# Optimization experiments

Hardware: AMD Instinct MI355X
Metric: run time of the kernel (lower is better)

Reference implementation:

```python
import jax, jax.numpy as jnp
import numpy as np

N_NODES = 100000
N_EDGES = 3200000
EMB = 128
HID = 128
N_CLASS = 10
N_SHAPE = 16
N_COLOR = 16
MAX_POS = 150000
N_GRAPH = 1024


def setup_inputs() -> dict:
    key = jax.random.key(0)
    ks = jax.random.split(key, 12)
    node_feats = jax.random.randint(ks[0], (N_NODES, 3), 0, N_SHAPE, dtype=jnp.int64 if jax.config.jax_enable_x64 else jnp.int32)
    edge_index = jax.random.randint(ks[1], (2, N_EDGES), 0, N_NODES)
    batch = jnp.sort(jax.random.randint(ks[2], (N_NODES,), 0, N_GRAPH))
    s = 0.02
    shape_emb = jax.random.normal(ks[3], (N_SHAPE, EMB), jnp.float32) * s
    color_emb = jax.random.normal(ks[4], (N_COLOR, EMB), jnp.float32) * s
    pos_emb = jax.random.normal(ks[5], (MAX_POS, EMB), jnp.float32) * s
    w1_l = jax.random.normal(ks[6], (HID, EMB), jnp.float32) / np.sqrt(EMB)
    b1_l = jnp.zeros((HID,), jnp.float32)
    w1_r = jax.random.normal(ks[7], (HID, EMB), jnp.float32) / np.sqrt(EMB)
    w2_l = jax.random.normal(ks[8], (HID, HID), jnp.float32) / np.sqrt(HID)
    b2_l = jnp.zeros((HID,), jnp.float32)
    w2_r = jax.random.normal(ks[9], (HID, HID), jnp.float32) / np.sqrt(HID)
    lin_w = jax.random.normal(ks[10], (N_CLASS, HID), jnp.float32) / np.sqrt(HID)
    lin_b = jnp.zeros((N_CLASS,), jnp.float32)
    return {"node_feats": node_feats, "edge_index": edge_index, "batch": batch,
            "shape_emb": shape_emb, "color_emb": color_emb, "pos_emb": pos_emb,
            "w1_l": w1_l, "b1_l": b1_l, "w1_r": w1_r,
            "w2_l": w2_l, "b2_l": b2_l, "w2_r": w2_r,
            "lin_w": lin_w, "lin_b": lin_b}


def _sage_conv(x, src, dst, deg_inv, w_l, b_l, w_r):
    # mean-aggregate neighbor features: gather x[src], scatter-add at dst, divide by degree
    msg_sum = jax.ops.segment_sum(x[src], dst, num_segments=N_NODES)  # [N, D]
    agg = msg_sum * deg_inv[:, None]
    # PyG SAGEConv: lin_l(aggr) + lin_r(x); bias lives in lin_l
    return agg @ w_l.T + b_l + x @ w_r.T


def reference(node_feats, edge_index, batch, shape_emb, color_emb, pos_emb,
              w1_l, b1_l, w1_r, w2_l, b2_l, w2_r, lin_w, lin_b):
    s, c, p = node_feats[:, 0], node_feats[:, 1], node_feats[:, 2]
    x = shape_emb[s] + color_emb[c] + pos_emb[p]            # [N, EMB]
    src, dst = edge_index[0], edge_index[1]
    deg = jax.ops.segment_sum(jnp.ones((N_EDGES,), x.dtype), dst, num_segments=N_NODES)
    deg_inv = jnp.where(deg > 0, 1.0 / jnp.maximum(deg, 1.0), 0.0)
    x = jax.nn.relu(_sage_conv(x, src, dst, deg_inv, w1_l, b1_l, w1_r))
    x = jax.nn.relu(_sage_conv(x, src, dst, deg_inv, w2_l, b2_l, w2_r))
    # global mean pool over graphs
    pooled_sum = jax.ops.segment_sum(x, batch, num_segments=N_GRAPH)  # [G, HID]
    counts = jax.ops.segment_sum(jnp.ones((N_NODES,), x.dtype), batch, num_segments=N_GRAPH)
    pooled = pooled_sum / jnp.maximum(counts, 1.0)[:, None]
    return pooled @ lin_w.T + lin_b                          # [G, N_CLASS]
```

## Files before the change

kernel.cpp:

```cpp
#include <hip/hip_runtime.h>

#define N_NODES 100000
#define N_EDGES 3200000
#define EMB 128
#define N_GRAPH 1024
#define N_CLASS 10
#define CAP 96

#define EPB 1280
#define NBLK_E (N_EDGES / EPB)
#define NBK 391
#define NTOT (NBK * NBLK_E)
#define SCAN_B 1024
#define NB_SCAN ((NTOT + SCAN_B - 1) / SCAN_B)

#define EMBED_BLKS (N_NODES * 16 / 256)
#define WCAT_BLKS 256

typedef unsigned int uint32;
typedef __attribute__((ext_vector_type(8))) short bf16x8;
typedef __attribute__((ext_vector_type(4))) float f32x4;
typedef __attribute__((ext_vector_type(2))) float f32x2;

__device__ inline unsigned short f2bf(float f) {
  unsigned u = __float_as_uint(f);
  u += 0x7fffu + ((u >> 16) & 1u);
  return (unsigned short)(u >> 16);
}
__device__ inline float bf2f(unsigned short s) {
  return __uint_as_float(((unsigned)s) << 16);
}
__device__ inline unsigned char f2fp8(float v) {
  return (unsigned char)(__builtin_amdgcn_cvt_pk_fp8_f32(v, v, 0, false) & 0xff);
}

__global__ __launch_bounds__(256) void k_hist(
    const int* __restrict__ dst, int* __restrict__ counts,
    const int* __restrict__ nf, const float* __restrict__ se,
    const float* __restrict__ ce, const float* __restrict__ pe,
    unsigned short* __restrict__ X, unsigned char* __restrict__ X8,
    const float* __restrict__ w1l, const float* __restrict__ w1r,
    const float* __restrict__ w2l, const float* __restrict__ w2r,
    unsigned short* __restrict__ wc1, unsigned short* __restrict__ wc2) {
  int b = blockIdx.x;
  int tid = threadIdx.x;
  if (b < NBLK_E) {
    __shared__ int h[NBK];
    for (int i = tid; i < NBK; i += 256) h[i] = 0;
    __syncthreads();
    int base = b * EPB;
#pragma unroll
    for (int it = 0; it < 5; ++it) {
      int d = dst[base + it * 256 + tid];
      atomicAdd(&h[d >> 8], 1);
    }
    __syncthreads();
    for (int i = tid; i < NBK; i += 256) counts[i * NBLK_E + b] = h[i];
  } else if (b < NBLK_E + EMBED_BLKS) {
    int gid = (b - NBLK_E) * 256 + tid;
    int node = gid >> 4;
    int q = (gid & 15) * 8;
    int s = nf[node * 3 + 0];
    int c = nf[node * 3 + 1];
    int p = nf[node * 3 + 2];
    const float* ps = se + s * EMB + q;
    const float* pc = ce + c * EMB + q;
    const float* pp = pe + p * EMB + q;
    float4 a0 = *(const float4*)ps, a1 = *(const float4*)(ps + 4);
    float4 b0 = *(const float4*)pc, b1 = *(const float4*)(pc + 4);
    float4 d0 = *(const float4*)pp, d1 = *(const float4*)(pp + 4);
    float r0 = a0.x + b0.x + d0.x, r1 = a0.y + b0.y + d0.y;
    float r2 = a0.z + b0.z + d0.z, r3 = a0.w + b0.w + d0.w;
    float r4 = a1.x + b1.x + d1.x, r5 = a1.y + b1.y + d1.y;
    float r6 = a1.z + b1.z + d1.z, r7 = a1.w + b1.w + d1.w;
    uint4 o;
    o.x = (uint32)f2bf(r0) | ((uint32)f2bf(r1) << 16);
    o.y = (uint32)f2bf(r2) | ((uint32)f2bf(r3) << 16);
    o.z = (uint32)f2bf(r4) | ((uint32)f2bf(r5) << 16);
    o.w = (uint32)f2bf(r6) | ((uint32)f2bf(r7) << 16);
    *(uint4*)(X + (size_t)node * EMB + q) = o;
    int w0 = __builtin_amdgcn_cvt_pk_fp8_f32(r0, r1, 0, false);
    w0 = __builtin_amdgcn_cvt_pk_fp8_f32(r2, r3, w0, true);
    int w1 = __builtin_amdgcn_cvt_pk_fp8_f32(r4, r5, 0, false);
    w1 = __builtin_amdgcn_cvt_pk_fp8_f32(r6, r7, w1, true);
    uint2 o8;
    o8.x = (uint32)w0;
    o8.y = (uint32)w1;
    *(uint2*)(X8 + (size_t)node * EMB + q) = o8;
  } else {
    int wb = b - (NBLK_E + EMBED_BLKS);
    const float* wl = (wb < 128) ? w1l : w2l;
    const float* wr = (wb < 128) ? w1r : w2r;
    unsigned short* wcat = (wb < 128) ? wc1 : wc2;
    int gid = (wb & 127) * 256 + tid;
    int j = gid >> 8;
    int k = gid & 255;
    float v = (k < EMB) ? wl[j * EMB + k] : wr[j * EMB + (k - EMB)];
    wcat[gid] = f2bf(v);
  }
}

__global__ void k_scan1(int* __restrict__ data, int* __restrict__ part) {
  __shared__ int t[SCAN_B];
  int tid = threadIdx.x;
  int gid = blockIdx.x * SCAN_B + tid;
  int v = (gid < NTOT) ? data[gid] : 0;
  t[tid] = v;
  __syncthreads();
  for (int s = 1; s < SCAN_B; s <<= 1) {
    int u = (tid >= s) ? t[tid - s] : 0;
    __syncthreads();
    t[tid] += u;
    __syncthreads();
  }
  if (gid < NTOT) data[gid] = t[tid] - v;
  if (tid == SCAN_B - 1) part[blockIdx.x] = t[tid];
}

__global__ void k_scan2(int* __restrict__ part) {
  __shared__ int t[1024];
  int tid = threadIdx.x;
  int v = (tid < NB_SCAN) ? part[tid] : 0;
  t[tid] = v;
  __syncthreads();
  for (int s = 1; s < 1024; s <<= 1) {
    int u = (tid >= s) ? t[tid - s] : 0;
    __syncthreads();
    t[tid] += u;
    __syncthreads();
  }
  if (tid < NB_SCAN) part[tid] = t[tid] - v;
}

__global__ __launch_bounds__(256) void k_part(const int* __restrict__ src,
                                              const int* __restrict__ dst,
                                              const int* __restrict__ counts,
                                              const int* __restrict__ part,
                                              uint32* __restrict__ psort) {
  __shared__ int h[NBK];
  __shared__ int scol[NBK];
  int b = blockIdx.x;
  int tid = threadIdx.x;
  for (int i = tid; i < NBK; i += 256) {
    h[i] = 0;
    int idx = i * NBLK_E + b;
    scol[i] = counts[idx] + part[idx >> 10];
  }
  __syncthreads();
  int base = b * EPB;
#pragma unroll
  for (int it = 0; it < 5; ++it) {
    int e = base + it * 256 + tid;
    int d = dst[e];
    int s = src[e];
    int r = atomicAdd(&h[d >> 8], 1);
    psort[scol[d >> 8] + r] = ((uint32)(d & 255) << 24) | (uint32)s;
  }
}

__global__ __launch_bounds__(256) void k_csr(const uint32* __restrict__ psort,
                                             const int* __restrict__ counts,
                                             const int* __restrict__ part,
                                             int* __restrict__ csrp,
                                             int* __restrict__ degi) {
  __shared__ int h[256];
  int b = blockIdx.x;
  int tid = threadIdx.x;
  h[tid] = 0;
  __syncthreads();
  int i0 = b * NBLK_E;
  int start = counts[i0] + part[i0 >> 10];
  int end = N_EDGES;
  if (b != NBK - 1) {
    int i1 = (b + 1) * NBLK_E;
    end = counts[i1] + part[i1 >> 10];
  }
  for (int e = start + tid; e < end; e += 256) {
    uint32 p = psort[e];
    int dl = (int)(p >> 24);
    int s = (int)(p & 0xFFFFFFu);
    int r = atomicAdd(&h[dl], 1);
    csrp[(size_t)(b * 256 + dl) * CAP + r] = s;
  }
  __syncthreads();
  int node = b * 256 + tid;
  if (node < N_NODES) degi[node] = h[tid];
}

__global__ __launch_bounds__(256) void k_agg(const unsigned char* __restrict__ in8,
                                             unsigned short* __restrict__ out,
                                             const int* __restrict__ degi,
                                             const int* __restrict__ csrp) {
  int grp = threadIdx.x >> 4;
  int l16 = threadIdx.x & 15;
  int node = blockIdx.x * 16 + grp;
  size_t start = (size_t)node * CAP;
  int cnt = degi[node];
  const unsigned char* base = in8 + l16 * 8;
  f32x2 a0 = {0.f, 0.f}, a1 = {0.f, 0.f}, a2 = {0.f, 0.f}, a3 = {0.f, 0.f};
  int i = 0;
  for (; i + 8 <= cnt; i += 8) {
    int s0 = csrp[start + i + 0];
    int s1 = csrp[start + i + 1];
    int s2 = csrp[start + i + 2];
    int s3 = csrp[start + i + 3];
    int s4 = csrp[start + i + 4];
    int s5 = csrp[start + i + 5];
    int s6 = csrp[start + i + 6];
    int s7 = csrp[start + i + 7];
    uint2 v0 = *(const uint2*)(base + (size_t)s0 * EMB);
    uint2 v1 = *(const uint2*)(base + (size_t)s1 * EMB);
    uint2 v2 = *(const uint2*)(base + (size_t)s2 * EMB);
    uint2 v3 = *(const uint2*)(base + (size_t)s3 * EMB);
    uint2 v4 = *(const uint2*)(base + (size_t)s4 * EMB);
    uint2 v5 = *(const uint2*)(base + (size_t)s5 * EMB);
    uint2 v6 = *(const uint2*)(base + (size_t)s6 * EMB);
    uint2 v7 = *(const uint2*)(base + (size_t)s7 * EMB);
#define ACC(v)                                                   \
    a0 += __builtin_amdgcn_cvt_pk_f32_fp8((int)v.x, false);      \
    a1 += __builtin_amdgcn_cvt_pk_f32_fp8((int)v.x, true);       \
    a2 += __builtin_amdgcn_cvt_pk_f32_fp8((int)v.y, false);      \
    a3 += __builtin_amdgcn_cvt_pk_f32_fp8((int)v.y, true);
    ACC(v0) ACC(v1) ACC(v2) ACC(v3) ACC(v4) ACC(v5) ACC(v6) ACC(v7)
  }
  for (; i < cnt; ++i) {
    int s = csrp[start + i];
    uint2 v = *(const uint2*)(base + (size_t)s * EMB);
    ACC(v)
  }
#undef ACC
  float di = cnt > 0 ? 1.0f / (float)cnt : 0.0f;
  uint4 o;
  o.x = (uint32)f2bf(a0.x * di) | ((uint32)f2bf(a0.y * di) << 16);
  o.y = (uint32)f2bf(a1.x * di) | ((uint32)f2bf(a1.y * di) << 16);
  o.z = (uint32)f2bf(a2.x * di) | ((uint32)f2bf(a2.y * di) << 16);
  o.w = (uint32)f2bf(a3.x * di) | ((uint32)f2bf(a3.y * di) << 16);
  *(uint4*)(out + (size_t)node * EMB + l16 * 8) = o;
}

__global__ __launch_bounds__(512) void k_gemm(const unsigned short* __restrict__ A,
                                              const unsigned short* __restrict__ S,
                                              const unsigned short* __restrict__ Wcat,
                                              const float* __restrict__ bias,
                                              unsigned short* __restrict__ out,
                                              unsigned char* __restrict__ out8) {
  __shared__ unsigned char ldsW[65536];
  int tid = threadIdx.x;
  {
    const uint4* w4 = (const uint4*)Wcat;
#pragma unroll
    for (int it = 0; it < 8; ++it) {
      int i = tid + it * 512;
      uint4 v = w4[i];
      unsigned a = (unsigned)i << 4;
      a ^= ((a >> 9) & 7u) << 4;
      *(uint4*)(ldsW + a) = v;
    }
  }
  __syncthreads();

  int wid = tid >> 6;
  int lane = tid & 63;
  int rows0 = blockIdx.x * 128 + wid * 16;
  int r = lane & 15;
  int khalf = lane >> 4;
  int arow = rows0 + r;
  if (arow > N_NODES - 1) arow = N_NODES - 1;
  const unsigned short* Abase = A + (size_t)arow * EMB + khalf * 8;
  const unsigned short* Sbase = S + (size_t)arow * EMB + khalf * 8;
  unsigned bswz = ((unsigned)(r & 7)) << 4;

  f32x4 acc[8] = {};
#pragma unroll
  for (int kc = 0; kc < 8; ++kc) {
    const unsigned short* p = (kc < 4) ? (Abase + kc * 32) : (Sbase + (kc - 4) * 32);
    bf16x8 a = *(const bf16x8*)p;
#pragma unroll
    for (int jc = 0; jc < 8; ++jc) {
      unsigned addr = (((unsigned)(jc * 16 + r)) << 9) + ((unsigned)kc << 6) +
                      ((unsigned)khalf << 4);
      bf16x8 b = *(const bf16x8*)(ldsW + (addr ^ bswz));
      acc[jc] = __builtin_amdgcn_mfma_f32_16x16x32_bf16(a, b, acc[jc], 0, 0, 0);
    }
  }

  int rbase = (lane >> 4) * 4;
#pragma unroll
  for (int jc = 0; jc < 8; ++jc) {
    int col = jc * 16 + r;
    float bv = bias[col];
#pragma unroll
    for (int q = 0; q < 4; ++q) {
      int row = rows0 + rbase + q;
      if (row < N_NODES) {
        float v = fmaxf(acc[jc][q] + bv, 0.f);
        out[(size_t)row * EMB + col] = f2bf(v);
        if (out8) out8[(size_t)row * EMB + col] = f2fp8(v);
      }
    }
  }
}

__global__ void k_pool(const unsigned short* __restrict__ h, const int* __restrict__ batch,
                       const float* __restrict__ lw, const float* __restrict__ lb,
                       float* __restrict__ out) {
  int g = blockIdx.x;
  int tid = threadIdx.x;
  int lo = 0, hi = N_NODES;
  while (lo < hi) {
    int mid = (lo + hi) >> 1;
    if (batch[mid] < g) lo = mid + 1; else hi = mid;
  }
  int lo2 = lo, hi2 = N_NODES;
  while (lo2 < hi2) {
    int mid = (lo2 + hi2) >> 1;
    if (batch[mid] < g + 1) lo2 = mid + 1; else hi2 = mid;
  }
  float sum = 0.f;
  for (int n = lo; n < lo2; ++n) sum += bf2f(h[(size_t)n * EMB + tid]);
  int cnt = lo2 - lo;
  float pooled = sum / fmaxf((float)cnt, 1.0f);
  __shared__ float pl[EMB];
  pl[tid] = pooled;
  __syncthreads();
  if (tid < N_CLASS) {
    float o = lb[tid];
    for (int d = 0; d < EMB; ++d) o += pl[d] * lw[tid * EMB + d];
    out[g * N_CLASS + tid] = o;
  }
}

extern "C" void kernel_launch(void* const* d_in, const int* in_sizes, int n_in,
                              void* d_out, int out_size, void* d_ws, size_t ws_size,
                              hipStream_t stream) {
  const int* nf = (const int*)d_in[0];
  const int* ei = (const int*)d_in[1];
  const int* batch = (const int*)d_in[2];
  const float* se = (const float*)d_in[3];
  const float* ce = (const float*)d_in[4];
  const float* pe = (const float*)d_in[5];
  const float* w1l = (const float*)d_in[6];
  const float* b1l = (const float*)d_in[7];
  const float* w1r = (const float*)d_in[8];
  const float* w2l = (const float*)d_in[9];
  const float* b2l = (const float*)d_in[10];
  const float* w2r = (const float*)d_in[11];
  const float* linw = (const float*)d_in[12];
  const float* linb = (const float*)d_in[13];
  float* out = (float*)d_out;

  char* ws = (char*)d_ws;
  size_t off = 0;
  auto alloc = [&](size_t bytes) {
    void* p = ws + off;
    off = (off + bytes + 255) & ~(size_t)255;
    return p;
  };
  unsigned short* X = (unsigned short*)alloc((size_t)N_NODES * EMB * 2);
  unsigned short* H = (unsigned short*)alloc((size_t)N_NODES * EMB * 2);
  unsigned short* X2 = (unsigned short*)alloc((size_t)N_NODES * EMB * 2);
  unsigned short* AGG = (unsigned short*)alloc((size_t)N_NODES * EMB * 2);
  unsigned char* X8 = (unsigned char*)alloc((size_t)N_NODES * EMB);
  unsigned char* H8 = (unsigned char*)alloc((size_t)N_NODES * EMB);
  unsigned short* WC1 = (unsigned short*)alloc((size_t)256 * EMB * 2);
  unsigned short* WC2 = (unsigned short*)alloc((size_t)256 * EMB * 2);
  int* degi = (int*)alloc((size_t)N_NODES * 4);
  int* counts = (int*)alloc((size_t)NTOT * 4);
  int* part = (int*)alloc((size_t)1024 * 4);
  uint32* psort = (uint32*)alloc((size_t)N_EDGES * 4);
  int* csrp = (int*)alloc((size_t)N_NODES * CAP * 4);

  const int* srcv = ei;
  const int* dstv = ei + N_EDGES;

  k_hist<<<NBLK_E + EMBED_BLKS + WCAT_BLKS, 256, 0, stream>>>(
      dstv, counts, nf, se, ce, pe, X, X8, w1l, w1r, w2l, w2r, WC1, WC2);
  k_scan1<<<NB_SCAN, SCAN_B, 0, stream>>>(counts, part);
  k_scan2<<<1, 1024, 0, stream>>>(part);
  k_part<<<NBLK_E, 256, 0, stream>>>(srcv, dstv, counts, part, psort);
  k_csr<<<NBK, 256, 0, stream>>>(psort, counts, part, csrp, degi);

  k_agg<<<N_NODES / 16 + 1, 256, 0, stream>>>(X8, AGG, degi, csrp);
  k_gemm<<<(N_NODES + 127) / 128, 512, 0, stream>>>(AGG, X, WC1, b1l, H, H8);
  k_agg<<<N_NODES / 16 + 1, 256, 0, stream>>>(H8, AGG, degi, csrp);
  k_gemm<<<(N_NODES + 127) / 128, 512, 0, stream>>>(AGG, H, WC2, b2l, X2, nullptr);
  k_pool<<<N_GRAPH, EMB, 0, stream>>>(X2, batch, linw, linb, out);
}
```

Measured before the change: 295.5 us.

## Split node feature matrices into four column-quarter planes for cache-friendly gathers

Node features (bf16 and fp8) are stored as four separate 32-column planes instead of row-major 128-wide rows. The aggregation kernel runs on a 2D grid with one grid dimension per plane, so each gather pass touches a working set a quarter the size, meant to fit better in L2/MALL. The GEMM reads and writes this planar layout, and index loads in the CSR and aggregation kernels become nontemporal. The cost is four times as many index reads, since each plane pass re-reads the CSR lists, plus smaller 4-byte gathers per lane.

```diff
diff --git a/kernel.cpp b/kernel.cpp
--- a/kernel.cpp
+++ b/kernel.cpp
@@ -6,6 +6,7 @@
 #define N_GRAPH 1024
 #define N_CLASS 10
 #define CAP 96
+#define QSZ ((size_t)N_NODES * 32)
 
 #define EPB 1280
 #define NBLK_E (N_EDGES / EPB)
@@ -60,6 +61,8 @@
     int gid = (b - NBLK_E) * 256 + tid;
     int node = gid >> 4;
     int q = (gid & 15) * 8;
+    int qq = (gid >> 2) & 3;
+    int o8 = (gid & 3) * 8;
     int s = nf[node * 3 + 0];
     int c = nf[node * 3 + 1];
     int p = nf[node * 3 + 2];
@@ -78,15 +81,15 @@
     o.y = (uint32)f2bf(r2) | ((uint32)f2bf(r3) << 16);
     o.z = (uint32)f2bf(r4) | ((uint32)f2bf(r5) << 16);
     o.w = (uint32)f2bf(r6) | ((uint32)f2bf(r7) << 16);
-    *(uint4*)(X + (size_t)node * EMB + q) = o;
+    *(uint4*)(X + (size_t)qq * QSZ + (size_t)node * 32 + o8) = o;
     int w0 = __builtin_amdgcn_cvt_pk_fp8_f32(r0, r1, 0, false);
     w0 = __builtin_amdgcn_cvt_pk_fp8_f32(r2, r3, w0, true);
     int w1 = __builtin_amdgcn_cvt_pk_fp8_f32(r4, r5, 0, false);
     w1 = __builtin_amdgcn_cvt_pk_fp8_f32(r6, r7, w1, true);
-    uint2 o8;
-    o8.x = (uint32)w0;
-    o8.y = (uint32)w1;
-    *(uint2*)(X8 + (size_t)node * EMB + q) = o8;
+    uint2 e8;
+    e8.x = (uint32)w0;
+    e8.y = (uint32)w1;
+    *(uint2*)(X8 + (size_t)qq * QSZ + (size_t)node * 32 + o8) = e8;
   } else {
     int wb = b - (NBLK_E + EMBED_BLKS);
     const float* wl = (wb < 128) ? w1l : w2l;
@@ -176,7 +179,7 @@
     end = counts[i1] + part[i1 >> 10];
   }
   for (int e = start + tid; e < end; e += 256) {
-    uint32 p = psort[e];
+    uint32 p = __builtin_nontemporal_load(&psort[e]);
     int dl = (int)(p >> 24);
     int s = (int)(p & 0xFFFFFFu);
     int r = atomicAdd(&h[dl], 1);
@@ -191,51 +194,48 @@
                                              unsigned short* __restrict__ out,
                                              const int* __restrict__ degi,
                                              const int* __restrict__ csrp) {
-  int grp = threadIdx.x >> 4;
-  int l16 = threadIdx.x & 15;
-  int node = blockIdx.x * 16 + grp;
+  int q = blockIdx.y;
+  int grp = threadIdx.x >> 3;
+  int l8 = threadIdx.x & 7;
+  int node = blockIdx.x * 32 + grp;
   size_t start = (size_t)node * CAP;
   int cnt = degi[node];
-  const unsigned char* base = in8 + l16 * 8;
-  f32x2 a0 = {0.f, 0.f}, a1 = {0.f, 0.f}, a2 = {0.f, 0.f}, a3 = {0.f, 0.f};
+  const unsigned char* base = in8 + (size_t)q * QSZ + l8 * 4;
+  f32x2 a0 = {0.f, 0.f}, a1 = {0.f, 0.f};
   int i = 0;
   for (; i + 8 <= cnt; i += 8) {
-    int s0 = csrp[start + i + 0];
-    int s1 = csrp[start + i + 1];
-    int s2 = csrp[start + i + 2];
-    int s3 = csrp[start + i + 3];
-    int s4 = csrp[start + i + 4];
-    int s5 = csrp[start + i + 5];
-    int s6 = csrp[start + i + 6];
-    int s7 = csrp[start + i + 7];
-    uint2 v0 = *(const uint2*)(base + (size_t)s0 * EMB);
-    uint2 v1 = *(const uint2*)(base + (size_t)s1 * EMB);
-    uint2 v2 = *(const uint2*)(base + (size_t)s2 * EMB);
-    uint2 v3 = *(const uint2*)(base + (size_t)s3 * EMB);
-    uint2 v4 = *(const uint2*)(base + (size_t)s4 * EMB);
-    uint2 v5 = *(const uint2*)(base + (size_t)s5 * EMB);
-    uint2 v6 = *(const uint2*)(base + (size_t)s6 * EMB);
-    uint2 v7 = *(const uint2*)(base + (size_t)s7 * EMB);
-#define ACC(v)                                                   \
-    a0 += __builtin_amdgcn_cvt_pk_f32_fp8((int)v.x, false);      \
-    a1 += __builtin_amdgcn_cvt_pk_f32_fp8((int)v.x, true);       \
-    a2 += __builtin_amdgcn_cvt_pk_f32_fp8((int)v.y, false);      \
-    a3 += __builtin_amdgcn_cvt_pk_f32_fp8((int)v.y, true);
+    int s0 = __builtin_nontemporal_load(&csrp[start + i + 0]);
+    int s1 = __builtin_nontemporal_load(&csrp[start + i + 1]);
+    int s2 = __builtin_nontemporal_load(&csrp[start + i + 2]);
+    int s3 = __builtin_nontemporal_load(&csrp[start + i + 3]);
+    int s4 = __builtin_nontemporal_load(&csrp[start + i + 4]);
+    int s5 = __builtin_nontemporal_load(&csrp[start + i + 5]);
+    int s6 = __builtin_nontemporal_load(&csrp[start + i + 6]);
+    int s7 = __builtin_nontemporal_load(&csrp[start + i + 7]);
+    uint32 v0 = *(const uint32*)(base + (size_t)s0 * 32);
+    uint32 v1 = *(const uint32*)(base + (size_t)s1 * 32);
+    uint32 v2 = *(const uint32*)(base + (size_t)s2 * 32);
+    uint32 v3 = *(const uint32*)(base + (size_t)s3 * 32);
+    uint32 v4 = *(const uint32*)(base + (size_t)s4 * 32);
+    uint32 v5 = *(const uint32*)(base + (size_t)s5 * 32);
+    uint32 v6 = *(const uint32*)(base + (size_t)s6 * 32);
+    uint32 v7 = *(const uint32*)(base + (size_t)s7 * 32);
+#define ACC(v)                                               \
+    a0 += __builtin_amdgcn_cvt_pk_f32_fp8((int)v, false);    \
+    a1 += __builtin_amdgcn_cvt_pk_f32_fp8((int)v, true);
     ACC(v0) ACC(v1) ACC(v2) ACC(v3) ACC(v4) ACC(v5) ACC(v6) ACC(v7)
   }
   for (; i < cnt; ++i) {
-    int s = csrp[start + i];
-    uint2 v = *(const uint2*)(base + (size_t)s * EMB);
+    int s = __builtin_nontemporal_load(&csrp[start + i]);
+    uint32 v = *(const uint32*)(base + (size_t)s * 32);
     ACC(v)
   }
 #undef ACC
   float di = cnt > 0 ? 1.0f / (float)cnt : 0.0f;
-  uint4 o;
+  uint2 o;
   o.x = (uint32)f2bf(a0.x * di) | ((uint32)f2bf(a0.y * di) << 16);
   o.y = (uint32)f2bf(a1.x * di) | ((uint32)f2bf(a1.y * di) << 16);
-  o.z = (uint32)f2bf(a2.x * di) | ((uint32)f2bf(a2.y * di) << 16);
-  o.w = (uint32)f2bf(a3.x * di) | ((uint32)f2bf(a3.y * di) << 16);
-  *(uint4*)(out + (size_t)node * EMB + l16 * 8) = o;
+  *(uint2*)(out + (size_t)q * QSZ + (size_t)node * 32 + l8 * 4) = o;
 }
 
 __global__ __launch_bounds__(512) void k_gemm(const unsigned short* __restrict__ A,
@@ -266,14 +266,14 @@
   int khalf = lane >> 4;
   int arow = rows0 + r;
   if (arow > N_NODES - 1) arow = N_NODES - 1;
-  const unsigned short* Abase = A + (size_t)arow * EMB + khalf * 8;
-  const unsigned short* Sbase = S + (size_t)arow * EMB + khalf * 8;
   unsigned bswz = ((unsigned)(r & 7)) << 4;
 
   f32x4 acc[8] = {};
 #pragma unroll
   for (int kc = 0; kc < 8; ++kc) {
-    const unsigned short* p = (kc < 4) ? (Abase + kc * 32) : (Sbase + (kc - 4) * 32);
+    const unsigned short* p =
+        (kc < 4) ? (A + (size_t)kc * QSZ + (size_t)arow * 32 + khalf * 8)
+                 : (S + (size_t)(kc - 4) * QSZ + (size_t)arow * 32 + khalf * 8);
     bf16x8 a = *(const bf16x8*)p;
 #pragma unroll
     for (int jc = 0; jc < 8; ++jc) {
@@ -289,13 +289,19 @@
   for (int jc = 0; jc < 8; ++jc) {
     int col = jc * 16 + r;
     float bv = bias[col];
+    int qq = col >> 5;
+    int co = col & 31;
 #pragma unroll
     for (int q = 0; q < 4; ++q) {
       int row = rows0 + rbase + q;
       if (row < N_NODES) {
         float v = fmaxf(acc[jc][q] + bv, 0.f);
-        out[(size_t)row * EMB + col] = f2bf(v);
-        if (out8) out8[(size_t)row * EMB + col] = f2fp8(v);
+        if (out8) {
+          out[(size_t)qq * QSZ + (size_t)row * 32 + co] = f2bf(v);
+          out8[(size_t)qq * QSZ + (size_t)row * 32 + co] = f2fp8(v);
+        } else {
+          out[(size_t)row * EMB + col] = f2bf(v);
+        }
       }
     }
   }
@@ -380,9 +386,9 @@
   k_part<<<NBLK_E, 256, 0, stream>>>(srcv, dstv, counts, part, psort);
   k_csr<<<NBK, 256, 0, stream>>>(psort, counts, part, csrp, degi);
 
-  k_agg<<<N_NODES / 16 + 1, 256, 0, stream>>>(X8, AGG, degi, csrp);
+  k_agg<<<dim3(N_NODES / 32, 4), 256, 0, stream>>>(X8, AGG, degi, csrp);
   k_gemm<<<(N_NODES + 127) / 128, 512, 0, stream>>>(AGG, X, WC1, b1l, H, H8);
-  k_agg<<<N_NODES / 16 + 1, 256, 0, stream>>>(H8, AGG, degi, csrp);
+  k_agg<<<dim3(N_NODES / 32, 4), 256, 0, stream>>>(H8, AGG, degi, csrp);
   k_gemm<<<(N_NODES + 127) / 128, 512, 0, stream>>>(AGG, H, WC2, b2l, X2, nullptr);
   k_pool<<<N_GRAPH, EMB, 0, stream>>>(X2, batch, linw, linb, out);
 }
```

New measurement: 464.5 us. +57.2%, slower.
